# Performance work log

Measured on AMD Instinct MI355X. Metric: run time of the kernel, lower is better.

Reference implementation:

```python
import jax, jax.numpy as jnp
import numpy as np

B, C, T = 64, 64, 1000   # batch, EEG channels (input_dim), timesteps
H = 512                   # hidden_dim
L = 3                     # num_layers
NC = 5                    # num_classes


def setup_inputs() -> dict:
    key = jax.random.key(0)
    ks = jax.random.split(key, 9)
    s_in = 1.0 / np.sqrt(H)  # torch LSTM init scale
    x = jax.random.normal(ks[0], (B, C, T), dtype=jnp.float32)
    W_ih0 = jax.random.uniform(ks[1], (4 * H, C), jnp.float32, -s_in, s_in)
    W_ih_rest = jax.random.uniform(ks[2], (L - 1, 4 * H, H), jnp.float32, -s_in, s_in)
    W_hh = jax.random.uniform(ks[3], (L, 4 * H, H), jnp.float32, -s_in, s_in)
    b_ih = jax.random.uniform(ks[4], (L, 4 * H), jnp.float32, -s_in, s_in)
    b_hh = jax.random.uniform(ks[5], (L, 4 * H), jnp.float32, -s_in, s_in)
    W_fc = jax.random.uniform(ks[6], (NC, H), jnp.float32, -s_in, s_in)
    b_fc = jax.random.uniform(ks[7], (NC,), jnp.float32, -s_in, s_in)
    return {"x": x, "W_ih0": W_ih0, "W_ih_rest": W_ih_rest, "W_hh": W_hh,
            "b_ih": b_ih, "b_hh": b_hh, "W_fc": W_fc, "b_fc": b_fc}


def _lstm_layer(x_tbc, W_ih, W_hh, b):
    """x_tbc: [T, B, in]. Returns (h_seq [T,B,H], h_T [B,H]). Gate order i,f,g,o (PyTorch)."""
    # Precompute input projections for all timesteps: [T, B, 4H]
    xg = jnp.einsum('tbi,gi->tbg', x_tbc, W_ih) + b

    def step(carry, xg_t):
        h, c = carry
        gates = xg_t + h @ W_hh.T  # [B, 4H]
        i, f, g, o = jnp.split(gates, 4, axis=-1)
        i, f, o = jax.nn.sigmoid(i), jax.nn.sigmoid(f), jax.nn.sigmoid(o)
        g = jnp.tanh(g)
        c = f * c + i * g
        h = o * jnp.tanh(c)
        return (h, c), h

    Bn = x_tbc.shape[1]
    h0 = jnp.zeros((Bn, H), x_tbc.dtype)
    (hT, _), h_seq = jax.lax.scan(step, (h0, h0), xg)
    return h_seq, hT


def reference(x, W_ih0, W_ih_rest, W_hh, b_ih, b_hh, W_fc, b_fc):
    # input_type='signal': [B, C, T] -> batch_first [B, T, C]; scan over time-major [T, B, C]
    seq = jnp.transpose(x, (2, 0, 1))  # [T, B, C]
    hT = None
    for l in range(L):
        W_ih = W_ih0 if l == 0 else W_ih_rest[l - 1]
        seq, hT = _lstm_layer(seq, W_ih, W_hh[l], b_ih[l] + b_hh[l])
    # dropout=0 (inference): identity
    return hT @ W_fc.T + b_fc  # [B, NC]
```

## Files before the change

kernel.cpp:

```cpp
#include <hip/hip_runtime.h>
#include <cstdint>

#define TB 64
#define TC 64
#define TT 1000
#define TH 512
#define NCLS 5
#define NTHR 512
#define STEPS 1002

#define H0_OFF 0
#define H1_OFF 8192
#define H2_OFF 16384
#define X_OFF  24576
#define SC_OFF 32768
#define SC_W   864
#define LDS_FLOATS (SC_OFF + 8 * SC_W)
#define LDS_BYTES  (LDS_FLOATS * 4)

__device__ __forceinline__ float sigf(float x) { return 1.0f / (1.0f + expf(-x)); }

__device__ __forceinline__ void pin4(float4& v) {
  asm volatile("" : "+v"(v.x), "+v"(v.y), "+v"(v.z), "+v"(v.w));
}

__device__ __forceinline__ void group_barrier(int* gb, int s, unsigned xcc,
                                              int occ_mine, int nxcd) {
  __syncthreads();
  if (threadIdx.x == 0) {
    const int t = s + 1;
    int a = __hip_atomic_fetch_add(gb + 16 + xcc, 1, __ATOMIC_RELAXED, __HIP_MEMORY_SCOPE_AGENT);
    if (a == occ_mine * t - 1) {
      __threadfence();
      int d = __hip_atomic_fetch_add(gb + 32, 1, __ATOMIC_RELAXED, __HIP_MEMORY_SCOPE_AGENT);
      if (d == nxcd * t - 1)
        __hip_atomic_fetch_add(gb + 40, 1, __ATOMIC_RELAXED, __HIP_MEMORY_SCOPE_AGENT);
    }
    while (__hip_atomic_load(gb + 40, __ATOMIC_RELAXED, __HIP_MEMORY_SCOPE_AGENT) < t)
      __builtin_amdgcn_s_sleep(1);
  }
  __syncthreads();
}

__device__ __forceinline__ void dot4(float& acc, const float4 a, const float4 b) {
  acc = fmaf(a.x, b.x, acc); acc = fmaf(a.y, b.y, acc);
  acc = fmaf(a.z, b.z, acc); acc = fmaf(a.w, b.w, acc);
}

__device__ __forceinline__ void gload_lds16_cg(const char* gsrc_lane, char* lds_base) {
  __builtin_amdgcn_global_load_lds(
      (const __attribute__((address_space(1))) unsigned int*)gsrc_lane,
      (__attribute__((address_space(3))) unsigned int*)lds_base, 16, 0, 0x11);
}

__global__ __launch_bounds__(NTHR) __attribute__((amdgpu_waves_per_eu(2, 2)))
void lstm_pipe(
    const float* __restrict__ x, const float* __restrict__ Wih0,
    const float* __restrict__ WihR, const float* __restrict__ Whh,
    const float* __restrict__ bih, const float* __restrict__ bhh,
    float* __restrict__ hbuf, int* __restrict__ bar)
{
  __shared__ float lds[LDS_FLOATS];
  const int tid = threadIdx.x;
  const int blk = blockIdx.x;
  const int grp = blk >> 6, slot = blk & 63;
  const int b_base = grp * 16;
  const int kk = tid >> 5;
  const int rt = tid & 31;
  const int g  = rt & 3;
  const int cl = rt >> 2;
  const int cell = slot * 8 + cl;
  const int row  = g * TH + cell;
  const int wv = tid >> 6;
  const int lane = tid & 63;

  int* gb = bar + grp * 64;

  float4 wx, wh0[8], w1a[8], w1b[8], w2a[8], w2b[8];
  wx = *(const float4*)(Wih0 + (size_t)row * TC + 4 * kk);
  pin4(wx);
  {
    const float* p0 = Whh  + (size_t)row * TH + 32 * kk;
    const float* p1 = WihR + (size_t)row * TH + 32 * kk;
    const float* p2 = Whh  + (size_t)(2048 + row) * TH + 32 * kk;
    const float* p3 = WihR + (size_t)(2048 + row) * TH + 32 * kk;
    const float* p4 = Whh  + (size_t)(4096 + row) * TH + 32 * kk;
#pragma unroll
    for (int i = 0; i < 8; ++i) {
      wh0[i] = *(const float4*)(p0 + 4 * i); pin4(wh0[i]);
      w1a[i] = *(const float4*)(p1 + 4 * i); pin4(w1a[i]);
      w1b[i] = *(const float4*)(p2 + 4 * i); pin4(w1b[i]);
      w2a[i] = *(const float4*)(p3 + 4 * i); pin4(w2a[i]);
      w2b[i] = *(const float4*)(p4 + 4 * i); pin4(w2b[i]);
    }
  }

  const int rl = tid >> 6;
  const int rc = (tid & 63) >> 3;
  const int rb = tid & 7;
  const int rcell = slot * 8 + rc;
  float4 bias_r = make_float4(0.f, 0.f, 0.f, 0.f);
  if (tid < 192) {
    bias_r.x = bih[rl * 2048 + rcell]        + bhh[rl * 2048 + rcell];
    bias_r.y = bih[rl * 2048 +  512 + rcell] + bhh[rl * 2048 +  512 + rcell];
    bias_r.z = bih[rl * 2048 + 1024 + rcell] + bhh[rl * 2048 + 1024 + rcell];
    bias_r.w = bih[rl * 2048 + 1536 + rcell] + bhh[rl * 2048 + 1536 + rcell];
  }
  float cst0 = 0.f, cst1 = 0.f;

  unsigned xcc = 0;
  int occ_mine = 0, nxcd = 0;
  if (tid == 0) {
    unsigned xr;
    asm volatile("s_getreg_b32 %0, hwreg(HW_REG_XCC_ID)" : "=s"(xr));
    xcc = xr & 7;
    __hip_atomic_fetch_add(gb + 8 + xcc, 1, __ATOMIC_RELAXED, __HIP_MEMORY_SCOPE_AGENT);
    int a = __hip_atomic_fetch_add(gb + 0, 1, __ATOMIC_RELAXED, __HIP_MEMORY_SCOPE_AGENT);
    if (a == 63)
      __hip_atomic_fetch_add(gb + 4, 1, __ATOMIC_RELAXED, __HIP_MEMORY_SCOPE_AGENT);
    while (__hip_atomic_load(gb + 4, __ATOMIC_RELAXED, __HIP_MEMORY_SCOPE_AGENT) < 1)
      __builtin_amdgcn_s_sleep(1);
#pragma unroll
    for (int i = 0; i < 8; ++i) {
      int o = __hip_atomic_load(gb + 8 + i, __ATOMIC_RELAXED, __HIP_MEMORY_SCOPE_AGENT);
      if (i == (int)xcc) occ_mine = o;
      if (o > 0) ++nxcd;
    }
  }
  __syncthreads();

  for (int s = 0; s < STEPS; ++s) {
    {
      const bool v0 = (s >= 1 && s <= 1000);
      const bool v1 = (s >= 2);
      const bool v2 = (s >= 3);
      const bool vc = ((s & 7) == 0 && s <= 999);
      if (v0) {
        const char* gp = (const char*)(hbuf + ((size_t)(0 + ((s - 1) & 1)) * TB + b_base) * TH);
        char* lb = (char*)lds + H0_OFF * 4;
#pragma unroll
        for (int i = 0; i < 4; ++i) {
          int off = wv * 4096 + i * 1024;
          gload_lds16_cg(gp + off + lane * 16, lb + off);
        }
      }
      if (v1) {
        const char* gp = (const char*)(hbuf + ((size_t)(2 + ((s - 2) & 1)) * TB + b_base) * TH);
        char* lb = (char*)lds + H1_OFF * 4;
#pragma unroll
        for (int i = 0; i < 4; ++i) {
          int off = wv * 4096 + i * 1024;
          gload_lds16_cg(gp + off + lane * 16, lb + off);
        }
      }
      if (v2) {
        const char* gp = (const char*)(hbuf + ((size_t)(4 + ((s - 3) & 1)) * TB + b_base) * TH);
        char* lb = (char*)lds + H2_OFF * 4;
#pragma unroll
        for (int i = 0; i < 4; ++i) {
          int off = wv * 4096 + i * 1024;
          gload_lds16_cg(gp + off + lane * 16, lb + off);
        }
      }
      if (vc) {
        const int e0 = tid, e1 = tid + NTHR;
        const float* q0 = x + (size_t)(b_base + (e0 >> 6)) * (TC * TT) + (size_t)(e0 & 63) * TT + s;
        const float* q1 = x + (size_t)(b_base + (e1 >> 6)) * (TC * TT) + (size_t)(e1 & 63) * TT + s;
        float4 xa0 = *(const float4*)(q0), xa1 = *(const float4*)(q0 + 4);
        float4 xb0 = *(const float4*)(q1), xb1 = *(const float4*)(q1 + 4);
        float* d0 = lds + X_OFF + (e0 >> 6) * 64 + (e0 & 63);
        float* d1 = lds + X_OFF + (e1 >> 6) * 64 + (e1 & 63);
        d0[0 * 1024] = xa0.x; d0[1 * 1024] = xa0.y; d0[2 * 1024] = xa0.z; d0[3 * 1024] = xa0.w;
        d0[4 * 1024] = xa1.x; d0[5 * 1024] = xa1.y; d0[6 * 1024] = xa1.z; d0[7 * 1024] = xa1.w;
        d1[0 * 1024] = xb0.x; d1[1 * 1024] = xb0.y; d1[2 * 1024] = xb0.z; d1[3 * 1024] = xb0.w;
        d1[4 * 1024] = xb1.x; d1[5 * 1024] = xb1.y; d1[6 * 1024] = xb1.z; d1[7 * 1024] = xb1.w;
      }
    }
    __syncthreads();

#pragma unroll
    for (int p = 0; p < 2; ++p) {
      float a0[8], a1[8], a2[8];
#pragma unroll
      for (int b = 0; b < 8; ++b) { a0[b] = 0.f; a1[b] = 0.f; a2[b] = 0.f; }
#pragma unroll
      for (int b = 0; b < 8; ++b) {
        const int bb = p * 8 + b;
        if (s <= 999) {
          float4 xf = *(const float4*)(lds + X_OFF + (s & 7) * 1024 + bb * 64 + 4 * kk);
          dot4(a0[b], wx, xf);
        }
        if (s >= 1 && s <= 1000) {
          const float* hb = lds + H0_OFF + bb * TH + 32 * kk;
#pragma unroll
          for (int c4 = 0; c4 < 2; ++c4) {
            float4 f0 = *(const float4*)(hb + 16 * c4 + 0);
            float4 f1 = *(const float4*)(hb + 16 * c4 + 4);
            float4 f2 = *(const float4*)(hb + 16 * c4 + 8);
            float4 f3 = *(const float4*)(hb + 16 * c4 + 12);
            if (s <= 999) {
              dot4(a0[b], wh0[4 * c4 + 0], f0); dot4(a0[b], wh0[4 * c4 + 1], f1);
              dot4(a0[b], wh0[4 * c4 + 2], f2); dot4(a0[b], wh0[4 * c4 + 3], f3);
            }
            dot4(a1[b], w1a[4 * c4 + 0], f0); dot4(a1[b], w1a[4 * c4 + 1], f1);
            dot4(a1[b], w1a[4 * c4 + 2], f2); dot4(a1[b], w1a[4 * c4 + 3], f3);
          }
        }
        if (s >= 2) {
          const float* hb = lds + H1_OFF + bb * TH + 32 * kk;
#pragma unroll
          for (int c4 = 0; c4 < 2; ++c4) {
            float4 f0 = *(const float4*)(hb + 16 * c4 + 0);
            float4 f1 = *(const float4*)(hb + 16 * c4 + 4);
            float4 f2 = *(const float4*)(hb + 16 * c4 + 8);
            float4 f3 = *(const float4*)(hb + 16 * c4 + 12);
            if (s <= 1000) {
              dot4(a1[b], w1b[4 * c4 + 0], f0); dot4(a1[b], w1b[4 * c4 + 1], f1);
              dot4(a1[b], w1b[4 * c4 + 2], f2); dot4(a1[b], w1b[4 * c4 + 3], f3);
            }
            dot4(a2[b], w2a[4 * c4 + 0], f0); dot4(a2[b], w2a[4 * c4 + 1], f1);
            dot4(a2[b], w2a[4 * c4 + 2], f2); dot4(a2[b], w2a[4 * c4 + 3], f3);
          }
        }
        if (s >= 3) {
          const float* hb = lds + H2_OFF + bb * TH + 32 * kk;
#pragma unroll
          for (int c4 = 0; c4 < 2; ++c4) {
            float4 f0 = *(const float4*)(hb + 16 * c4 + 0);
            float4 f1 = *(const float4*)(hb + 16 * c4 + 4);
            float4 f2 = *(const float4*)(hb + 16 * c4 + 8);
            float4 f3 = *(const float4*)(hb + 16 * c4 + 12);
            dot4(a2[b], w2b[4 * c4 + 0], f0); dot4(a2[b], w2b[4 * c4 + 1], f1);
            dot4(a2[b], w2b[4 * c4 + 2], f2); dot4(a2[b], w2b[4 * c4 + 3], f3);
          }
        }
      }
#pragma unroll
      for (int b = 0; b < 8; ++b) {
        a0[b] += __shfl_xor(a0[b], 32, 64);
        a1[b] += __shfl_xor(a1[b], 32, 64);
        a2[b] += __shfl_xor(a2[b], 32, 64);
      }
      if ((tid & 32) == 0) {
        float* sb = lds + SC_OFF + wv * SC_W + cl * 36 + g;
#pragma unroll
        for (int b = 0; b < 8; ++b) {
          sb[4 * b]       = a0[b];
          sb[288 + 4 * b] = a1[b];
          sb[576 + 4 * b] = a2[b];
        }
      }
      __syncthreads();
      if (tid < 192) {
        const int tl = s - rl;
        if (tl >= 0 && tl < TT) {
          float sx = 0.f, sy = 0.f, sz = 0.f, sw = 0.f;
          const float* sb = lds + SC_OFF + rl * 288 + rc * 36 + 4 * rb;
#pragma unroll
          for (int w8 = 0; w8 < 8; ++w8) {
            float4 v = *(const float4*)(sb + w8 * SC_W);
            sx += v.x; sy += v.y; sz += v.z; sw += v.w;
          }
          float ii = sigf(sx + bias_r.x);
          float ff = sigf(sy + bias_r.y);
          float gg = tanhf(sz + bias_r.z);
          float oo = sigf(sw + bias_r.w);
          float cprev = p ? cst1 : cst0;
          float cc = (tl == 0) ? ii * gg : fmaf(ff, cprev, ii * gg);
          if (p) cst1 = cc; else cst0 = cc;
          float hh = oo * tanhf(cc);
          hbuf[((size_t)(rl * 2 + (tl & 1)) * TB + b_base + p * 8 + rb) * TH + rcell] = hh;
        }
      }
      __syncthreads();
    }
    group_barrier(gb, s, xcc, occ_mine, nxcd);
  }
}

__global__ void fc_kernel(const float* __restrict__ hbuf, const float* __restrict__ Wfc,
                          const float* __restrict__ bfc, float* __restrict__ out) {
  int bb = blockIdx.x, lane = threadIdx.x;
  const float* h = hbuf + ((size_t)5 * TB + bb) * TH;
  for (int n = 0; n < NCLS; ++n) {
    float s = 0.f;
    for (int k = lane; k < TH; k += 64) s = fmaf(h[k], Wfc[n * TH + k], s);
    for (int off = 32; off > 0; off >>= 1) s += __shfl_down(s, off, 64);
    if (lane == 0) out[bb * NCLS + n] = s + bfc[n];
  }
}

extern "C" void kernel_launch(void* const* d_in, const int* in_sizes, int n_in,
                              void* d_out, int out_size, void* d_ws, size_t ws_size,
                              hipStream_t stream) {
  const float* x    = (const float*)d_in[0];
  const float* Wih0 = (const float*)d_in[1];
  const float* WihR = (const float*)d_in[2];
  const float* Whh  = (const float*)d_in[3];
  const float* bih  = (const float*)d_in[4];
  const float* bhh  = (const float*)d_in[5];
  const float* Wfc  = (const float*)d_in[6];
  const float* bfc  = (const float*)d_in[7];
  float* out = (float*)d_out;

  char* ws = (char*)d_ws;
  int*   bar  = (int*)ws;
  float* hbuf = (float*)(ws + 1024);

  hipMemsetAsync(bar, 0, 1024, stream);
  lstm_pipe<<<256, NTHR, 0, stream>>>(x, Wih0, WihR, Whh, bih, bhh, hbuf, bar);
  fc_kernel<<<TB, 64, 0, stream>>>(hbuf, Wfc, bfc, out);
}
```

Baseline: 17.16 ms.

## Merge batch halves into one pass, flatten grid barrier, load x per step

The two 8-batch passes per timestep are merged into a single pass over all 16 batches. This removes two of the three block-wide barriers per step and widens the gate-reduction stage from 192 to 384 threads. The grid barrier drops its second-level counter, so every block now polls the shared per-XCC arrival sum directly. The x input is loaded as a single scalar each step instead of as an 8-step staged chunk, which frees LDS for a larger scratch buffer. The cost is twice as many accumulator registers (48 floats) under a tight waves-per-EU limit, which may cause spills, plus more scalar global loads of x.

After: 20.18 ms. 1.18x slower.

```diff
diff --git a/kernel.cpp b/kernel.cpp
--- a/kernel.cpp
+++ b/kernel.cpp
@@ -13,8 +13,8 @@
 #define H1_OFF 8192
 #define H2_OFF 16384
 #define X_OFF  24576
-#define SC_OFF 32768
-#define SC_W   864
+#define SC_OFF 25600
+#define SC_W   1632
 #define LDS_FLOATS (SC_OFF + 8 * SC_W)
 #define LDS_BYTES  (LDS_FLOATS * 4)
 
@@ -32,11 +32,9 @@
     int a = __hip_atomic_fetch_add(gb + 16 + xcc, 1, __ATOMIC_RELAXED, __HIP_MEMORY_SCOPE_AGENT);
     if (a == occ_mine * t - 1) {
       __threadfence();
-      int d = __hip_atomic_fetch_add(gb + 32, 1, __ATOMIC_RELAXED, __HIP_MEMORY_SCOPE_AGENT);
-      if (d == nxcd * t - 1)
-        __hip_atomic_fetch_add(gb + 40, 1, __ATOMIC_RELAXED, __HIP_MEMORY_SCOPE_AGENT);
-    }
-    while (__hip_atomic_load(gb + 40, __ATOMIC_RELAXED, __HIP_MEMORY_SCOPE_AGENT) < t)
+      __hip_atomic_fetch_add(gb + 32, 1, __ATOMIC_RELAXED, __HIP_MEMORY_SCOPE_AGENT);
+    }
+    while (__hip_atomic_load(gb + 32, __ATOMIC_RELAXED, __HIP_MEMORY_SCOPE_AGENT) < nxcd * t)
       __builtin_amdgcn_s_sleep(1);
   }
   __syncthreads();
@@ -95,18 +93,19 @@
     }
   }
 
-  const int rl = tid >> 6;
-  const int rc = (tid & 63) >> 3;
-  const int rb = tid & 7;
+  const int rl = tid >> 7;
+  const int ridx = tid & 127;
+  const int rc = ridx >> 4;
+  const int rb = ridx & 15;
   const int rcell = slot * 8 + rc;
   float4 bias_r = make_float4(0.f, 0.f, 0.f, 0.f);
-  if (tid < 192) {
+  if (tid < 384) {
     bias_r.x = bih[rl * 2048 + rcell]        + bhh[rl * 2048 + rcell];
     bias_r.y = bih[rl * 2048 +  512 + rcell] + bhh[rl * 2048 +  512 + rcell];
     bias_r.z = bih[rl * 2048 + 1024 + rcell] + bhh[rl * 2048 + 1024 + rcell];
     bias_r.w = bih[rl * 2048 + 1536 + rcell] + bhh[rl * 2048 + 1536 + rcell];
   }
-  float cst0 = 0.f, cst1 = 0.f;
+  float cst = 0.f;
 
   unsigned xcc = 0;
   int occ_mine = 0, nxcd = 0;
@@ -134,7 +133,6 @@
       const bool v0 = (s >= 1 && s <= 1000);
       const bool v1 = (s >= 2);
       const bool v2 = (s >= 3);
-      const bool vc = ((s & 7) == 0 && s <= 999);
       if (v0) {
         const char* gp = (const char*)(hbuf + ((size_t)(0 + ((s - 1) & 1)) * TB + b_base) * TH);
         char* lb = (char*)lds + H0_OFF * 4;
@@ -162,36 +160,28 @@
           gload_lds16_cg(gp + off + lane * 16, lb + off);
         }
       }
-      if (vc) {
+      if (s <= 999) {
         const int e0 = tid, e1 = tid + NTHR;
-        const float* q0 = x + (size_t)(b_base + (e0 >> 6)) * (TC * TT) + (size_t)(e0 & 63) * TT + s;
-        const float* q1 = x + (size_t)(b_base + (e1 >> 6)) * (TC * TT) + (size_t)(e1 & 63) * TT + s;
-        float4 xa0 = *(const float4*)(q0), xa1 = *(const float4*)(q0 + 4);
-        float4 xb0 = *(const float4*)(q1), xb1 = *(const float4*)(q1 + 4);
-        float* d0 = lds + X_OFF + (e0 >> 6) * 64 + (e0 & 63);
-        float* d1 = lds + X_OFF + (e1 >> 6) * 64 + (e1 & 63);
-        d0[0 * 1024] = xa0.x; d0[1 * 1024] = xa0.y; d0[2 * 1024] = xa0.z; d0[3 * 1024] = xa0.w;
-        d0[4 * 1024] = xa1.x; d0[5 * 1024] = xa1.y; d0[6 * 1024] = xa1.z; d0[7 * 1024] = xa1.w;
-        d1[0 * 1024] = xb0.x; d1[1 * 1024] = xb0.y; d1[2 * 1024] = xb0.z; d1[3 * 1024] = xb0.w;
-        d1[4 * 1024] = xb1.x; d1[5 * 1024] = xb1.y; d1[6 * 1024] = xb1.z; d1[7 * 1024] = xb1.w;
+        float xs0 = x[(size_t)(b_base + (e0 >> 6)) * (TC * TT) + (size_t)(e0 & 63) * TT + s];
+        float xs1 = x[(size_t)(b_base + (e1 >> 6)) * (TC * TT) + (size_t)(e1 & 63) * TT + s];
+        lds[X_OFF + e0] = xs0;
+        lds[X_OFF + e1] = xs1;
       }
     }
     __syncthreads();
 
-#pragma unroll
-    for (int p = 0; p < 2; ++p) {
-      float a0[8], a1[8], a2[8];
-#pragma unroll
-      for (int b = 0; b < 8; ++b) { a0[b] = 0.f; a1[b] = 0.f; a2[b] = 0.f; }
-#pragma unroll
-      for (int b = 0; b < 8; ++b) {
-        const int bb = p * 8 + b;
+    {
+      float a0[16], a1[16], a2[16];
+#pragma unroll
+      for (int b = 0; b < 16; ++b) { a0[b] = 0.f; a1[b] = 0.f; a2[b] = 0.f; }
+#pragma unroll
+      for (int b = 0; b < 16; ++b) {
         if (s <= 999) {
-          float4 xf = *(const float4*)(lds + X_OFF + (s & 7) * 1024 + bb * 64 + 4 * kk);
+          float4 xf = *(const float4*)(lds + X_OFF + b * TC + 4 * kk);
           dot4(a0[b], wx, xf);
         }
         if (s >= 1 && s <= 1000) {
-          const float* hb = lds + H0_OFF + bb * TH + 32 * kk;
+          const float* hb = lds + H0_OFF + b * TH + 32 * kk;
 #pragma unroll
           for (int c4 = 0; c4 < 2; ++c4) {
             float4 f0 = *(const float4*)(hb + 16 * c4 + 0);
@@ -207,7 +197,7 @@
           }
         }
         if (s >= 2) {
-          const float* hb = lds + H1_OFF + bb * TH + 32 * kk;
+          const float* hb = lds + H1_OFF + b * TH + 32 * kk;
 #pragma unroll
           for (int c4 = 0; c4 < 2; ++c4) {
             float4 f0 = *(const float4*)(hb + 16 * c4 + 0);
@@ -223,7 +213,7 @@
           }
         }
         if (s >= 3) {
-          const float* hb = lds + H2_OFF + bb * TH + 32 * kk;
+          const float* hb = lds + H2_OFF + b * TH + 32 * kk;
 #pragma unroll
           for (int c4 = 0; c4 < 2; ++c4) {
             float4 f0 = *(const float4*)(hb + 16 * c4 + 0);
@@ -236,43 +226,42 @@
         }
       }
 #pragma unroll
-      for (int b = 0; b < 8; ++b) {
+      for (int b = 0; b < 16; ++b) {
         a0[b] += __shfl_xor(a0[b], 32, 64);
         a1[b] += __shfl_xor(a1[b], 32, 64);
         a2[b] += __shfl_xor(a2[b], 32, 64);
       }
       if ((tid & 32) == 0) {
-        float* sb = lds + SC_OFF + wv * SC_W + cl * 36 + g;
-#pragma unroll
-        for (int b = 0; b < 8; ++b) {
-          sb[4 * b]       = a0[b];
-          sb[288 + 4 * b] = a1[b];
-          sb[576 + 4 * b] = a2[b];
-        }
-      }
-      __syncthreads();
-      if (tid < 192) {
-        const int tl = s - rl;
-        if (tl >= 0 && tl < TT) {
-          float sx = 0.f, sy = 0.f, sz = 0.f, sw = 0.f;
-          const float* sb = lds + SC_OFF + rl * 288 + rc * 36 + 4 * rb;
-#pragma unroll
-          for (int w8 = 0; w8 < 8; ++w8) {
-            float4 v = *(const float4*)(sb + w8 * SC_W);
-            sx += v.x; sy += v.y; sz += v.z; sw += v.w;
-          }
-          float ii = sigf(sx + bias_r.x);
-          float ff = sigf(sy + bias_r.y);
-          float gg = tanhf(sz + bias_r.z);
-          float oo = sigf(sw + bias_r.w);
-          float cprev = p ? cst1 : cst0;
-          float cc = (tl == 0) ? ii * gg : fmaf(ff, cprev, ii * gg);
-          if (p) cst1 = cc; else cst0 = cc;
-          float hh = oo * tanhf(cc);
-          hbuf[((size_t)(rl * 2 + (tl & 1)) * TB + b_base + p * 8 + rb) * TH + rcell] = hh;
-        }
-      }
-      __syncthreads();
+        float* sb = lds + SC_OFF + wv * SC_W + cl * 68 + g;
+#pragma unroll
+        for (int b = 0; b < 16; ++b) {
+          sb[4 * b]        = a0[b];
+          sb[544 + 4 * b]  = a1[b];
+          sb[1088 + 4 * b] = a2[b];
+        }
+      }
+    }
+    __syncthreads();
+
+    if (tid < 384) {
+      const int tl = s - rl;
+      if (tl >= 0 && tl < TT) {
+        float sx = 0.f, sy = 0.f, sz = 0.f, sw = 0.f;
+        const float* sbr = lds + SC_OFF + rl * 544 + rc * 68 + 4 * rb;
+#pragma unroll
+        for (int w8 = 0; w8 < 8; ++w8) {
+          float4 v = *(const float4*)(sbr + w8 * SC_W);
+          sx += v.x; sy += v.y; sz += v.z; sw += v.w;
+        }
+        float ii = sigf(sx + bias_r.x);
+        float ff = sigf(sy + bias_r.y);
+        float gg = tanhf(sz + bias_r.z);
+        float oo = sigf(sw + bias_r.w);
+        float cc = (tl == 0) ? ii * gg : fmaf(ff, cst, ii * gg);
+        cst = cc;
+        float hh = oo * tanhf(cc);
+        hbuf[((size_t)(rl * 2 + (tl & 1)) * TB + b_base + rb) * TH + rcell] = hh;
+      }
     }
     group_barrier(gb, s, xcc, occ_mine, nxcd);
   }
```
